# Optimization experiments

Measured on AMD Instinct MI355X. Metric: run time of the kernel, lower is better.

Reference implementation:

```python
import jax, jax.numpy as jnp
import numpy as np

B, N, D = 4, 4096, 1024
STD = 1.0 / D

def setup_inputs() -> dict:
    key = jax.random.key(0)
    ks = jax.random.split(key, 6)
    return {
        "x_real": jax.random.normal(ks[0], (B, N, D), dtype=jnp.float32),
        "x_imag": jax.random.normal(ks[1], (B, N, D), dtype=jnp.float32),
        "w_query_real": jax.random.normal(ks[2], (D, D), dtype=jnp.float32) * STD,
        "w_query_imag": jax.random.normal(ks[3], (D, D), dtype=jnp.float32) * STD,
        "w_key": jax.random.normal(ks[4], (D, D), dtype=jnp.float32) * STD,
        "w_value": jax.random.normal(ks[5], (D, D), dtype=jnp.float32) * STD,
    }

def reference(x_real, x_imag, w_query_real, w_query_imag, w_key, w_value):
    # query gate: (x.real @ Wqr) * (x.imag @ Wqi)  -> [b, n, e]
    query = jnp.einsum('bnd,de->bne', x_real, w_query_real) * \
            jnp.einsum('bnd,de->bne', x_imag, w_query_imag)
    key = jnp.einsum('bnd,de->bne', x_real, w_key)      # [b, n, d]
    value = jnp.einsum('bnd,de->bne', x_imag, w_value)  # [b, n, e]
    # linear-attention style reduction over sequence dim n
    kv_attn = jnp.einsum('bnd,bne->bde', key, value)    # [b, d, e]
    # dropout with p=0.0 (eval / identity)
    bffn = jnp.einsum('bnd,bde->bne', query, kv_attn)   # [b, n, e]
    return bffn
```

## Files before the change

### kernel.cpp

```cpp
#include <hip/hip_runtime.h>
#include <stdint.h>

typedef unsigned short ushort_t;
typedef __attribute__((ext_vector_type(8))) short bf16x8;
typedef __attribute__((ext_vector_type(4))) float f32x4;

__device__ __forceinline__ ushort_t f2bf(float f) {
  union { float f; uint32_t u; } v; v.f = f;
  uint32_t u = v.u;
  u += 0x7FFFu + ((u >> 16) & 1u);
  return (ushort_t)(u >> 16);
}
__device__ __forceinline__ float bf2f(ushort_t h) {
  union { uint32_t u; float f; } v; v.u = ((uint32_t)h) << 16;
  return v.f;
}
__device__ __forceinline__ void gl2lds16(const void* g, void* l) {
  __builtin_amdgcn_global_load_lds(
      (__attribute__((address_space(1))) void*)(uintptr_t)g,
      (__attribute__((address_space(3))) void*)(uint32_t)(uintptr_t)l,
      16, 0, 0);
}

__device__ __forceinline__ void gemm256x128(
    const ushort_t* __restrict__ A, int lda,
    const ushort_t* __restrict__ Bt, int ldb,
    int m0, int n0, int K, char* __restrict__ smem,
    f32x4 (&acc)[4][4]) {
  const int t = threadIdx.x;
  const int lane = t & 63, wid = t >> 6;
  const int wm = wid >> 1, wn = wid & 1;
  const int lr = lane & 15, lq = lane >> 4;
  const int nt = K >> 5;

  const int rowS = t >> 2;
  const int kgS = (t & 3) ^ ((t >> 3) & 3);
  const ushort_t* a0 = A + (size_t)(m0 + rowS) * lda + kgS * 8;
  const ushort_t* a1 = a0 + (size_t)128 * lda;
  const ushort_t* b0 = Bt + (size_t)(n0 + rowS) * ldb + kgS * 8;
  const int d0 = t * 16;

  const int o = lr * 64 + ((lq ^ ((lr >> 1) & 3)) << 4);
  const int aW = wm * 4096;
  const int bW = 16384 + wn * 4096;

#define STAGE(tt, buf) do { \
    char* s = smem + (buf); \
    gl2lds16(a0 + (tt) * 32, s + d0); \
    gl2lds16(a1 + (tt) * 32, s + 8192 + d0); \
    gl2lds16(b0 + (tt) * 32, s + 16384 + d0); \
  } while (0)

  bf16x8 aF[4], bF[4];

  STAGE(0, 0);
  for (int tt = 0; tt < nt; ++tt) {
    asm volatile("s_waitcnt vmcnt(0) lgkmcnt(0)\n\ts_barrier" ::: "memory");
    const int cb = (tt & 1) ? 24576 : 0;
    if (tt + 1 < nt) STAGE(tt + 1, (tt & 1) ? 0 : 24576);
    const char* base = smem + cb;
    #pragma unroll
    for (int mi = 0; mi < 4; ++mi)
      aF[mi] = *(const bf16x8*)(base + aW + mi * 1024 + o);
    #pragma unroll
    for (int ni = 0; ni < 4; ++ni)
      bF[ni] = *(const bf16x8*)(base + bW + ni * 1024 + o);
    __builtin_amdgcn_s_setprio(1);
    #pragma unroll
    for (int mi = 0; mi < 4; ++mi)
      #pragma unroll
      for (int ni = 0; ni < 4; ++ni)
        acc[mi][ni] = __builtin_amdgcn_mfma_f32_16x16x32_bf16(aF[mi], bF[ni], acc[mi][ni], 0, 0, 0);
    __builtin_amdgcn_s_setprio(0);
  }
#undef STAGE
}

template <bool GATE>
__global__ __launch_bounds__(512, 4) void proj8(
    const ushort_t* __restrict__ X, const ushort_t* __restrict__ Wt,
    ushort_t* __restrict__ Cq, ushort_t* __restrict__ Ct,
    const ushort_t* __restrict__ gate) {
  extern __shared__ char smem[];
  const int bid = blockIdx.x;
  const int xcd = bid & 7, i = bid >> 3;
  const int m0 = (xcd * 8 + (i >> 4)) * 256;
  const int n0 = (i & 15) * 128;
  f32x4 acc[4][4] = {};
  gemm256x128(X, 1024, Wt, 1024, m0, n0, 1024, smem, acc);

  const int t = threadIdx.x, lane = t & 63, wid = t >> 6;
  const int wm = wid >> 1, wn = wid & 1;
  const int lr = lane & 15, lq = lane >> 4;

  if (n0 < 1024) {
    #pragma unroll
    for (int mi = 0; mi < 4; ++mi) {
      int rbase = m0 + wm * 64 + mi * 16 + lq * 4;
      #pragma unroll
      for (int ni = 0; ni < 4; ++ni) {
        int c = n0 + wn * 64 + ni * 16 + lr;
        #pragma unroll
        for (int r = 0; r < 4; ++r) {
          float v = acc[mi][ni][r];
          if constexpr (GATE) v *= bf2f(gate[(size_t)(rbase + r) * 1024 + c]);
          Cq[(size_t)(rbase + r) * 1024 + c] = f2bf(v);
        }
      }
    }
  } else {
    const int b = m0 >> 12, nseq0 = m0 & 4095;
    #pragma unroll
    for (int p = 0; p < 2; ++p) {
      __syncthreads();
      #pragma unroll
      for (int mi = 0; mi < 4; ++mi) {
        int ns0 = wm * 64 + mi * 16 + lq * 4;
        int nc = ns0 >> 3, half8 = (ns0 >> 2) & 1;
        #pragma unroll
        for (int nib = 0; nib < 2; ++nib) {
          int ni = p * 2 + nib;
          int row = wn * 32 + nib * 16 + lr;
          ushort4 u = make_ushort4(f2bf(acc[mi][ni][0]), f2bf(acc[mi][ni][1]),
                                   f2bf(acc[mi][ni][2]), f2bf(acc[mi][ni][3]));
          *(ushort4*)(smem + row * 512 + ((nc ^ (row & 31)) * 16) + half8 * 8) = u;
        }
      }
      __syncthreads();
      #pragma unroll
      for (int j = 0; j < 4; ++j) {
        int g = j * 512 + t;
        int r = g >> 5, nc2 = g & 31;
        bf16x8 v = *(const bf16x8*)(smem + r * 512 + ((nc2 ^ (r & 31)) * 16));
        int d = n0 - 1024 + (r >> 5) * 64 + p * 32 + ((r >> 4) & 1) * 16 + (r & 15);
        *(bf16x8*)&Ct[(((size_t)(b * 1024 + d)) << 12) + nseq0 + nc2 * 8] = v;
      }
    }
  }
}

__global__ __launch_bounds__(512, 4) void kv8(
    const ushort_t* __restrict__ VT, const ushort_t* __restrict__ KT,
    ushort_t* __restrict__ P) {
  extern __shared__ char smem[];
  const int bid = blockIdx.x;
  const int xcd = bid & 7, i = bid >> 3;
  const int z = xcd * 2 + (i >> 5);
  const int mn = i & 31;
  const int m0 = (mn >> 3) * 256, n0 = (mn & 7) * 128;
  const int b = z & 3, s = z >> 2;
  const ushort_t* A = VT + ((size_t)b << 22) + s * 1024;
  const ushort_t* Bt = KT + ((size_t)b << 22) + s * 1024;
  f32x4 acc[4][4] = {};
  gemm256x128(A, 4096, Bt, 4096, m0, n0, 1024, smem, acc);

  const int t = threadIdx.x, lane = t & 63, wid = t >> 6;
  const int wm = wid >> 1, wn = wid & 1;
  const int lr = lane & 15, lq = lane >> 4;
  ushort_t* C = P + ((size_t)z << 20);
  #pragma unroll
  for (int mi = 0; mi < 4; ++mi) {
    int rbase = m0 + wm * 64 + mi * 16 + lq * 4;
    #pragma unroll
    for (int ni = 0; ni < 4; ++ni) {
      int c = n0 + wn * 64 + ni * 16 + lr;
      #pragma unroll
      for (int r = 0; r < 4; ++r)
        C[(size_t)(rbase + r) * 1024 + c] = f2bf(acc[mi][ni][r]);
    }
  }
}

__global__ __launch_bounds__(256) void kv_reduce(const ushort_t* __restrict__ P,
                                                 ushort_t* __restrict__ KVT) {
  size_t e4 = ((size_t)blockIdx.x * 256 + threadIdx.x) * 4;
  int b = (int)(e4 >> 20);
  size_t j = e4 & ((1u << 20) - 1);
  float s0 = 0.f, s1 = 0.f, s2 = 0.f, s3 = 0.f;
  #pragma unroll
  for (int sp = 0; sp < 4; ++sp) {
    ushort4 v = *(const ushort4*)(P + ((size_t)(sp * 4 + b) << 20) + j);
    s0 += bf2f(v.x); s1 += bf2f(v.y); s2 += bf2f(v.z); s3 += bf2f(v.w);
  }
  *(ushort4*)&KVT[e4] = make_ushort4(f2bf(s0), f2bf(s1), f2bf(s2), f2bf(s3));
}

__global__ __launch_bounds__(512, 4) void fin8(
    const ushort_t* __restrict__ Q, const ushort_t* __restrict__ KVT,
    float* __restrict__ Out) {
  extern __shared__ char smem[];
  const int bid = blockIdx.x;
  const int xcd = bid & 7, i = bid >> 3;
  const int m0 = (xcd * 8 + (i >> 3)) * 256;
  const int n0 = (i & 7) * 128;
  const int b = m0 >> 12;
  f32x4 acc[4][4] = {};
  gemm256x128(Q, 1024, KVT + ((size_t)b << 20), 1024, m0, n0, 1024, smem, acc);

  const int t = threadIdx.x, lane = t & 63, wid = t >> 6;
  const int wm = wid >> 1, wn = wid & 1;
  const int lr = lane & 15, lq = lane >> 4;
  #pragma unroll
  for (int mi = 0; mi < 4; ++mi) {
    int rbase = m0 + wm * 64 + mi * 16 + lq * 4;
    #pragma unroll
    for (int ni = 0; ni < 4; ++ni) {
      int c = n0 + wn * 64 + ni * 16 + lr;
      #pragma unroll
      for (int r = 0; r < 4; ++r)
        Out[(size_t)(rbase + r) * 1024 + c] = acc[mi][ni][r];
    }
  }
}

__global__ __launch_bounds__(256) void prep(
    const float* __restrict__ xr, const float* __restrict__ xi,
    const float* w0, const float* w1, const float* w2, const float* w3,
    ushort_t* __restrict__ xrb, ushort_t* __restrict__ xib,
    ushort_t* o0, ushort_t* o1, ushort_t* o2, ushort_t* o3) {
  const int bid = blockIdx.x;
  const int t = threadIdx.x;
  if (bid < 4096) {
    __shared__ float tile[32][33];
    const float* W; ushort_t* O;
    switch (bid >> 10) {
      case 0: W = w0; O = o0; break;
      case 1: W = w1; O = o1; break;
      case 2: W = w2; O = o2; break;
      default: W = w3; O = o3; break;
    }
    const int within = bid & 1023;
    const int bx = (within & 31) * 32, by = (within >> 5) * 32;
    const int tx = t & 31, ty = t >> 5;
    #pragma unroll
    for (int k = 0; k < 32; k += 8)
      tile[ty + k][tx] = W[(size_t)(by + ty + k) * 1024 + bx + tx];
    __syncthreads();
    #pragma unroll
    for (int k = 0; k < 32; k += 8)
      O[(size_t)(bx + ty + k) * 1024 + by + tx] = f2bf(tile[tx][ty + k]);
  } else {
    const size_t T = 16u * 1024u * 1024u;
    size_t e = ((size_t)(bid - 4096) * 256 + t) * 8;
    const float* src; ushort_t* dst;
    if (e < T) { src = xr + e; dst = xrb + e; }
    else       { src = xi + (e - T); dst = xib + (e - T); }
    float4 f0 = *(const float4*)src;
    float4 f1 = *(const float4*)(src + 4);
    ushort4 u0 = make_ushort4(f2bf(f0.x), f2bf(f0.y), f2bf(f0.z), f2bf(f0.w));
    ushort4 u1 = make_ushort4(f2bf(f1.x), f2bf(f1.y), f2bf(f1.z), f2bf(f1.w));
    *(ushort4*)dst = u0;
    *(ushort4*)(dst + 4) = u1;
  }
}

extern "C" void kernel_launch(void* const* d_in, const int* in_sizes, int n_in,
                              void* d_out, int out_size, void* d_ws, size_t ws_size,
                              hipStream_t stream) {
  const float* xr  = (const float*)d_in[0];
  const float* xi  = (const float*)d_in[1];
  const float* wqr = (const float*)d_in[2];
  const float* wqi = (const float*)d_in[3];
  const float* wk  = (const float*)d_in[4];
  const float* wv  = (const float*)d_in[5];

  char* ws = (char*)d_ws;
  const size_t MB = 1024ull * 1024ull;
  ushort_t* WtQR = (ushort_t*)(ws + 0 * MB);
  ushort_t* WtK  = (ushort_t*)(ws + 2 * MB);
  ushort_t* WtQI = (ushort_t*)(ws + 4 * MB);
  ushort_t* WtV  = (ushort_t*)(ws + 6 * MB);
  ushort_t* Xrb  = (ushort_t*)(ws + 8 * MB);
  ushort_t* Xib  = (ushort_t*)(ws + 40 * MB);
  ushort_t* KT   = (ushort_t*)(ws + 72 * MB);
  ushort_t* Q    = (ushort_t*)(ws + 104 * MB);
  ushort_t* VT   = (ushort_t*)(ws + 8 * MB);
  ushort_t* KVT  = (ushort_t*)(ws + 40 * MB);
  ushort_t* QR   = (ushort_t*)d_out;
  ushort_t* KVP  = (ushort_t*)d_out;

  static bool inited = false;
  if (!inited) {
    inited = true;
    hipFuncSetAttribute((const void*)&proj8<false>, hipFuncAttributeMaxDynamicSharedMemorySize, 49152);
    hipFuncSetAttribute((const void*)&proj8<true>,  hipFuncAttributeMaxDynamicSharedMemorySize, 49152);
    hipFuncSetAttribute((const void*)&kv8,          hipFuncAttributeMaxDynamicSharedMemorySize, 49152);
    hipFuncSetAttribute((const void*)&fin8,         hipFuncAttributeMaxDynamicSharedMemorySize, 49152);
  }

  prep<<<20480, 256, 0, stream>>>(xr, xi, wqr, wqi, wk, wv,
                                  Xrb, Xib, WtQR, WtQI, WtK, WtV);
  proj8<false><<<1024, 512, 49152, stream>>>(Xrb, WtQR, QR, KT, nullptr);
  proj8<true><<<1024, 512, 49152, stream>>>(Xib, WtQI, Q, VT, QR);
  kv8<<<512, 512, 49152, stream>>>(VT, KT, KVP);
  kv_reduce<<<4096, 256, 0, stream>>>(KVP, KVT);
  fin8<<<512, 512, 49152, stream>>>(Q, KVT, (float*)d_out);
}
```

Before: 420.4 us.

## Reassociate key-value product via Gram matrix of inputs and fuse query projections

Result: slower. 438.9 us (+4.4%).

```diff
diff --git a/kernel.cpp b/kernel.cpp
--- a/kernel.cpp
+++ b/kernel.cpp
@@ -22,24 +22,24 @@
       16, 0, 0);
 }
 
+
+template <bool F32OUT>
 __device__ __forceinline__ void gemm256x128(
     const ushort_t* __restrict__ A, int lda,
     const ushort_t* __restrict__ Bt, int ldb,
     int m0, int n0, int K, char* __restrict__ smem,
     f32x4 (&acc)[4][4]) {
   const int t = threadIdx.x;
-  const int lane = t & 63, wid = t >> 6;
-  const int wm = wid >> 1, wn = wid & 1;
-  const int lr = lane & 15, lq = lane >> 4;
   const int nt = K >> 5;
-
   const int rowS = t >> 2;
   const int kgS = (t & 3) ^ ((t >> 3) & 3);
   const ushort_t* a0 = A + (size_t)(m0 + rowS) * lda + kgS * 8;
   const ushort_t* a1 = a0 + (size_t)128 * lda;
   const ushort_t* b0 = Bt + (size_t)(n0 + rowS) * ldb + kgS * 8;
   const int d0 = t * 16;
-
+  const int lane = t & 63, wid = t >> 6;
+  const int wm = wid >> 1, wn = wid & 1;
+  const int lr = lane & 15, lq = lane >> 4;
   const int o = lr * 64 + ((lq ^ ((lr >> 1) & 3)) << 4);
   const int aW = wm * 4096;
   const int bW = 16384 + wn * 4096;
@@ -52,7 +52,6 @@
   } while (0)
 
   bf16x8 aF[4], bF[4];
-
   STAGE(0, 0);
   for (int tt = 0; tt < nt; ++tt) {
     asm volatile("s_waitcnt vmcnt(0) lgkmcnt(0)\n\ts_barrier" ::: "memory");
@@ -76,72 +75,90 @@
 #undef STAGE
 }
 
-template <bool GATE>
-__global__ __launch_bounds__(512, 4) void proj8(
-    const ushort_t* __restrict__ X, const ushort_t* __restrict__ Wt,
-    ushort_t* __restrict__ Cq, ushort_t* __restrict__ Ct,
-    const ushort_t* __restrict__ gate) {
+__global__ __launch_bounds__(512, 2) void gq(
+    const ushort_t* __restrict__ Xr, const ushort_t* __restrict__ Xi,
+    const ushort_t* __restrict__ Wr, const ushort_t* __restrict__ Wi,
+    ushort_t* __restrict__ Q) {
   extern __shared__ char smem[];
   const int bid = blockIdx.x;
   const int xcd = bid & 7, i = bid >> 3;
-  const int m0 = (xcd * 8 + (i >> 4)) * 256;
-  const int n0 = (i & 15) * 128;
-  f32x4 acc[4][4] = {};
-  gemm256x128(X, 1024, Wt, 1024, m0, n0, 1024, smem, acc);
-
-  const int t = threadIdx.x, lane = t & 63, wid = t >> 6;
+  const int m0 = (xcd * 8 + (i >> 3)) * 256;
+  const int n0 = (i & 7) * 128;
+  const int t = threadIdx.x;
+  const int lane = t & 63, wid = t >> 6;
   const int wm = wid >> 1, wn = wid & 1;
   const int lr = lane & 15, lq = lane >> 4;
 
-  if (n0 < 1024) {
+  const int rowS = t >> 2;
+  const int kgS = (t & 3) ^ ((t >> 3) & 3);
+  const ushort_t* ar0 = Xr + (size_t)(m0 + rowS) * 1024 + kgS * 8;
+  const ushort_t* ar1 = ar0 + (size_t)128 * 1024;
+  const ushort_t* ai0 = Xi + (size_t)(m0 + rowS) * 1024 + kgS * 8;
+  const ushort_t* ai1 = ai0 + (size_t)128 * 1024;
+  const ushort_t* br0 = Wr + (size_t)(n0 + rowS) * 1024 + kgS * 8;
+  const ushort_t* bi0 = Wi + (size_t)(n0 + rowS) * 1024 + kgS * 8;
+  const int d0 = t * 16;
+  const int o = lr * 64 + ((lq ^ ((lr >> 1) & 3)) << 4);
+  const int aW = wm * 4096;
+  const int bW = wn * 4096;
+
+#define STAGEQ(tt, buf) do { \
+    char* s = smem + (buf); \
+    gl2lds16(ar0 + (tt) * 32, s + d0); \
+    gl2lds16(ar1 + (tt) * 32, s + 8192 + d0); \
+    gl2lds16(ai0 + (tt) * 32, s + 16384 + d0); \
+    gl2lds16(ai1 + (tt) * 32, s + 24576 + d0); \
+    gl2lds16(br0 + (tt) * 32, s + 32768 + d0); \
+    gl2lds16(bi0 + (tt) * 32, s + 40960 + d0); \
+  } while (0)
+
+  f32x4 accR[4][4] = {}, accI[4][4] = {};
+  bf16x8 aR[4], aI[4], bR[4], bI[4];
+
+  STAGEQ(0, 0);
+  for (int tt = 0; tt < 32; ++tt) {
+    asm volatile("s_waitcnt vmcnt(0) lgkmcnt(0)\n\ts_barrier" ::: "memory");
+    const int cb = (tt & 1) ? 49152 : 0;
+    if (tt + 1 < 32) STAGEQ(tt + 1, (tt & 1) ? 0 : 49152);
+    const char* base = smem + cb;
     #pragma unroll
     for (int mi = 0; mi < 4; ++mi) {
-      int rbase = m0 + wm * 64 + mi * 16 + lq * 4;
+      aR[mi] = *(const bf16x8*)(base + aW + mi * 1024 + o);
+      aI[mi] = *(const bf16x8*)(base + 16384 + aW + mi * 1024 + o);
+    }
+    #pragma unroll
+    for (int ni = 0; ni < 4; ++ni) {
+      bR[ni] = *(const bf16x8*)(base + 32768 + bW + ni * 1024 + o);
+      bI[ni] = *(const bf16x8*)(base + 40960 + bW + ni * 1024 + o);
+    }
+    __builtin_amdgcn_s_setprio(1);
+    #pragma unroll
+    for (int mi = 0; mi < 4; ++mi)
       #pragma unroll
       for (int ni = 0; ni < 4; ++ni) {
-        int c = n0 + wn * 64 + ni * 16 + lr;
-        #pragma unroll
-        for (int r = 0; r < 4; ++r) {
-          float v = acc[mi][ni][r];
-          if constexpr (GATE) v *= bf2f(gate[(size_t)(rbase + r) * 1024 + c]);
-          Cq[(size_t)(rbase + r) * 1024 + c] = f2bf(v);
-        }
+        accR[mi][ni] = __builtin_amdgcn_mfma_f32_16x16x32_bf16(aR[mi], bR[ni], accR[mi][ni], 0, 0, 0);
+        accI[mi][ni] = __builtin_amdgcn_mfma_f32_16x16x32_bf16(aI[mi], bI[ni], accI[mi][ni], 0, 0, 0);
       }
-    }
-  } else {
-    const int b = m0 >> 12, nseq0 = m0 & 4095;
-    #pragma unroll
-    for (int p = 0; p < 2; ++p) {
-      __syncthreads();
-      #pragma unroll
-      for (int mi = 0; mi < 4; ++mi) {
-        int ns0 = wm * 64 + mi * 16 + lq * 4;
-        int nc = ns0 >> 3, half8 = (ns0 >> 2) & 1;
-        #pragma unroll
-        for (int nib = 0; nib < 2; ++nib) {
-          int ni = p * 2 + nib;
-          int row = wn * 32 + nib * 16 + lr;
-          ushort4 u = make_ushort4(f2bf(acc[mi][ni][0]), f2bf(acc[mi][ni][1]),
-                                   f2bf(acc[mi][ni][2]), f2bf(acc[mi][ni][3]));
-          *(ushort4*)(smem + row * 512 + ((nc ^ (row & 31)) * 16) + half8 * 8) = u;
-        }
-      }
-      __syncthreads();
-      #pragma unroll
-      for (int j = 0; j < 4; ++j) {
-        int g = j * 512 + t;
-        int r = g >> 5, nc2 = g & 31;
-        bf16x8 v = *(const bf16x8*)(smem + r * 512 + ((nc2 ^ (r & 31)) * 16));
-        int d = n0 - 1024 + (r >> 5) * 64 + p * 32 + ((r >> 4) & 1) * 16 + (r & 15);
-        *(bf16x8*)&Ct[(((size_t)(b * 1024 + d)) << 12) + nseq0 + nc2 * 8] = v;
-      }
-    }
-  }
-}
-
-__global__ __launch_bounds__(512, 4) void kv8(
-    const ushort_t* __restrict__ VT, const ushort_t* __restrict__ KT,
-    ushort_t* __restrict__ P) {
+    __builtin_amdgcn_s_setprio(0);
+  }
+#undef STAGEQ
+
+  #pragma unroll
+  for (int mi = 0; mi < 4; ++mi) {
+    int rbase = m0 + wm * 64 + mi * 16 + lq * 4;
+    #pragma unroll
+    for (int ni = 0; ni < 4; ++ni) {
+      int c = n0 + wn * 64 + ni * 16 + lr;
+      #pragma unroll
+      for (int r = 0; r < 4; ++r)
+        Q[(size_t)(rbase + r) * 1024 + c] = f2bf(accR[mi][ni][r] * accI[mi][ni][r]);
+    }
+  }
+}
+
+__global__ __launch_bounds__(512, 4) void gpart(
+    const ushort_t* __restrict__ XrT, const ushort_t* __restrict__ XiT,
+    float* __restrict__ P) {
   extern __shared__ char smem[];
   const int bid = blockIdx.x;
   const int xcd = bid & 7, i = bid >> 3;
@@ -149,15 +166,15 @@
   const int mn = i & 31;
   const int m0 = (mn >> 3) * 256, n0 = (mn & 7) * 128;
   const int b = z & 3, s = z >> 2;
-  const ushort_t* A = VT + ((size_t)b << 22) + s * 1024;
-  const ushort_t* Bt = KT + ((size_t)b << 22) + s * 1024;
+  const ushort_t* A = XrT + ((size_t)b << 22) + s * 1024;
+  const ushort_t* Bt = XiT + ((size_t)b << 22) + s * 1024;
   f32x4 acc[4][4] = {};
-  gemm256x128(A, 4096, Bt, 4096, m0, n0, 1024, smem, acc);
+  gemm256x128<true>(A, 4096, Bt, 4096, m0, n0, 1024, smem, acc);
 
   const int t = threadIdx.x, lane = t & 63, wid = t >> 6;
   const int wm = wid >> 1, wn = wid & 1;
   const int lr = lane & 15, lq = lane >> 4;
-  ushort_t* C = P + ((size_t)z << 20);
+  float* C = P + ((size_t)z << 20);
   #pragma unroll
   for (int mi = 0; mi < 4; ++mi) {
     int rbase = m0 + wm * 64 + mi * 16 + lq * 4;
@@ -166,23 +183,95 @@
       int c = n0 + wn * 64 + ni * 16 + lr;
       #pragma unroll
       for (int r = 0; r < 4; ++r)
-        C[(size_t)(rbase + r) * 1024 + c] = f2bf(acc[mi][ni][r]);
-    }
-  }
-}
-
-__global__ __launch_bounds__(256) void kv_reduce(const ushort_t* __restrict__ P,
-                                                 ushort_t* __restrict__ KVT) {
+        C[(size_t)(rbase + r) * 1024 + c] = acc[mi][ni][r];
+    }
+  }
+}
+
+__global__ __launch_bounds__(256) void g_reduce(const float* __restrict__ P,
+                                                ushort_t* __restrict__ G) {
   size_t e4 = ((size_t)blockIdx.x * 256 + threadIdx.x) * 4;
   int b = (int)(e4 >> 20);
   size_t j = e4 & ((1u << 20) - 1);
   float s0 = 0.f, s1 = 0.f, s2 = 0.f, s3 = 0.f;
   #pragma unroll
   for (int sp = 0; sp < 4; ++sp) {
-    ushort4 v = *(const ushort4*)(P + ((size_t)(sp * 4 + b) << 20) + j);
-    s0 += bf2f(v.x); s1 += bf2f(v.y); s2 += bf2f(v.z); s3 += bf2f(v.w);
-  }
-  *(ushort4*)&KVT[e4] = make_ushort4(f2bf(s0), f2bf(s1), f2bf(s2), f2bf(s3));
+    float4 v = *(const float4*)(P + ((size_t)(sp * 4 + b) << 20) + j);
+    s0 += v.x; s1 += v.y; s2 += v.z; s3 += v.w;
+  }
+  *(ushort4*)&G[e4] = make_ushort4(f2bf(s0), f2bf(s1), f2bf(s2), f2bf(s3));
+}
+
+__global__ __launch_bounds__(256, 4) void gemm1k(
+    const ushort_t* __restrict__ Abase, int aStride,
+    const ushort_t* __restrict__ Btbase, int btStride,
+    ushort_t* __restrict__ Cbase) {
+  extern __shared__ char smem[];
+  const int bid = blockIdx.x;
+  const int b = bid >> 6, mn = bid & 63;
+  const int m0 = (mn >> 3) * 128, n0 = (mn & 7) * 128;
+  const ushort_t* A = Abase + (size_t)b * (size_t)aStride;
+  const ushort_t* Bt = Btbase + (size_t)b * (size_t)btStride;
+
+  const int t = threadIdx.x;
+  const int lane = t & 63, wid = t >> 6;
+  const int wm = wid >> 1, wn = wid & 1;
+  const int lr = lane & 15, lq = lane >> 4;
+  const int rowS = t >> 2;
+  const int kgS = (t & 3) ^ ((t >> 3) & 3);
+  const ushort_t* a0 = A + (size_t)(m0 + rowS) * 1024 + kgS * 8;
+  const ushort_t* a1 = a0 + (size_t)64 * 1024;
+  const ushort_t* b0 = Bt + (size_t)(n0 + rowS) * 1024 + kgS * 8;
+  const ushort_t* b1 = b0 + (size_t)64 * 1024;
+  const int d0 = t * 16, d1 = 4096 + t * 16;
+  const int o = lr * 64 + ((lq ^ ((lr >> 1) & 3)) << 4);
+  const int aW = wm * 4096;
+  const int bW = 8192 + wn * 4096;
+
+#define STG1(tt, buf) do { \
+    char* s = smem + (buf); \
+    gl2lds16(a0 + (tt) * 32, s + d0); \
+    gl2lds16(a1 + (tt) * 32, s + d1); \
+    gl2lds16(b0 + (tt) * 32, s + 8192 + d0); \
+    gl2lds16(b1 + (tt) * 32, s + 8192 + d1); \
+  } while (0)
+
+  f32x4 acc[4][4] = {};
+  bf16x8 aF[4], bF[4];
+  STG1(0, 0);
+  for (int tt = 0; tt < 32; ++tt) {
+    asm volatile("s_waitcnt vmcnt(0) lgkmcnt(0)\n\ts_barrier" ::: "memory");
+    const int cb = (tt & 1) ? 16384 : 0;
+    if (tt + 1 < 32) STG1(tt + 1, (tt & 1) ? 0 : 16384);
+    const char* base = smem + cb;
+    #pragma unroll
+    for (int mi = 0; mi < 4; ++mi)
+      aF[mi] = *(const bf16x8*)(base + aW + mi * 1024 + o);
+    #pragma unroll
+    for (int ni = 0; ni < 4; ++ni)
+      bF[ni] = *(const bf16x8*)(base + bW + ni * 1024 + o);
+    __builtin_amdgcn_s_setprio(1);
+    #pragma unroll
+    for (int mi = 0; mi < 4; ++mi)
+      #pragma unroll
+      for (int ni = 0; ni < 4; ++ni)
+        acc[mi][ni] = __builtin_amdgcn_mfma_f32_16x16x32_bf16(aF[mi], bF[ni], acc[mi][ni], 0, 0, 0);
+    __builtin_amdgcn_s_setprio(0);
+  }
+#undef STG1
+
+  ushort_t* C = Cbase + ((size_t)b << 20);
+  #pragma unroll
+  for (int mi = 0; mi < 4; ++mi) {
+    int rbase = m0 + wm * 64 + mi * 16 + lq * 4;
+    #pragma unroll
+    for (int ni = 0; ni < 4; ++ni) {
+      int c = n0 + wn * 64 + ni * 16 + lr;
+      #pragma unroll
+      for (int r = 0; r < 4; ++r)
+        C[(size_t)(rbase + r) * 1024 + c] = f2bf(acc[mi][ni][r]);
+    }
+  }
 }
 
 __global__ __launch_bounds__(512, 4) void fin8(
@@ -195,7 +284,7 @@
   const int n0 = (i & 7) * 128;
   const int b = m0 >> 12;
   f32x4 acc[4][4] = {};
-  gemm256x128(Q, 1024, KVT + ((size_t)b << 20), 1024, m0, n0, 1024, smem, acc);
+  gemm256x128<true>(Q, 1024, KVT + ((size_t)b << 20), 1024, m0, n0, 1024, smem, acc);
 
   const int t = threadIdx.x, lane = t & 63, wid = t >> 6;
   const int wm = wid >> 1, wn = wid & 1;
@@ -213,15 +302,17 @@
   }
 }
 
-__global__ __launch_bounds__(256) void prep(
+__global__ __launch_bounds__(256) void prep2(
     const float* __restrict__ xr, const float* __restrict__ xi,
     const float* w0, const float* w1, const float* w2, const float* w3,
     ushort_t* __restrict__ xrb, ushort_t* __restrict__ xib,
+    ushort_t* __restrict__ xrT, ushort_t* __restrict__ xiT,
     ushort_t* o0, ushort_t* o1, ushort_t* o2, ushort_t* o3) {
   const int bid = blockIdx.x;
   const int t = threadIdx.x;
+  __shared__ float tile[32][33];
+  const int tx = t & 31, ty = t >> 5;
   if (bid < 4096) {
-    __shared__ float tile[32][33];
     const float* W; ushort_t* O;
     switch (bid >> 10) {
       case 0: W = w0; O = o0; break;
@@ -231,7 +322,6 @@
     }
     const int within = bid & 1023;
     const int bx = (within & 31) * 32, by = (within >> 5) * 32;
-    const int tx = t & 31, ty = t >> 5;
     #pragma unroll
     for (int k = 0; k < 32; k += 8)
       tile[ty + k][tx] = W[(size_t)(by + ty + k) * 1024 + bx + tx];
@@ -240,17 +330,27 @@
     for (int k = 0; k < 32; k += 8)
       O[(size_t)(bx + ty + k) * 1024 + by + tx] = f2bf(tile[tx][ty + k]);
   } else {
-    const size_t T = 16u * 1024u * 1024u;
-    size_t e = ((size_t)(bid - 4096) * 256 + t) * 8;
-    const float* src; ushort_t* dst;
-    if (e < T) { src = xr + e; dst = xrb + e; }
-    else       { src = xi + (e - T); dst = xib + (e - T); }
-    float4 f0 = *(const float4*)src;
-    float4 f1 = *(const float4*)(src + 4);
-    ushort4 u0 = make_ushort4(f2bf(f0.x), f2bf(f0.y), f2bf(f0.z), f2bf(f0.w));
-    ushort4 u1 = make_ushort4(f2bf(f1.x), f2bf(f1.y), f2bf(f1.z), f2bf(f1.w));
-    *(ushort4*)dst = u0;
-    *(ushort4*)(dst + 4) = u1;
+    const int xb = bid - 4096;
+    const int tensor = xb >> 14;
+    const int within = xb & 16383;
+    const int by = (within >> 5) * 32;
+    const int bx = (within & 31) * 32;
+    const float* src = tensor ? xi : xr;
+    ushort_t* dstS = tensor ? xib : xrb;
+    ushort_t* dstT = tensor ? xiT : xrT;
+    #pragma unroll
+    for (int k = 0; k < 32; k += 8) {
+      float v = src[(size_t)(by + ty + k) * 1024 + bx + tx];
+      tile[ty + k][tx] = v;
+      dstS[(size_t)(by + ty + k) * 1024 + bx + tx] = f2bf(v);
+    }
+    __syncthreads();
+    const int b = by >> 12;
+    const int nn = by & 4095;
+    #pragma unroll
+    for (int k = 0; k < 32; k += 8)
+      dstT[((size_t)b << 22) + (size_t)(bx + ty + k) * 4096 + nn + tx] =
+          f2bf(tile[tx][ty + k]);
   }
 }
 
@@ -267,32 +367,34 @@
   char* ws = (char*)d_ws;
   const size_t MB = 1024ull * 1024ull;
   ushort_t* WtQR = (ushort_t*)(ws + 0 * MB);
-  ushort_t* WtK  = (ushort_t*)(ws + 2 * MB);
-  ushort_t* WtQI = (ushort_t*)(ws + 4 * MB);
+  ushort_t* WtQI = (ushort_t*)(ws + 2 * MB);
+  ushort_t* WtK  = (ushort_t*)(ws + 4 * MB);
   ushort_t* WtV  = (ushort_t*)(ws + 6 * MB);
-  ushort_t* Xrb  = (ushort_t*)(ws + 8 * MB);
-  ushort_t* Xib  = (ushort_t*)(ws + 40 * MB);
-  ushort_t* KT   = (ushort_t*)(ws + 72 * MB);
-  ushort_t* Q    = (ushort_t*)(ws + 104 * MB);
-  ushort_t* VT   = (ushort_t*)(ws + 8 * MB);
-  ushort_t* KVT  = (ushort_t*)(ws + 40 * MB);
-  ushort_t* QR   = (ushort_t*)d_out;
-  ushort_t* KVP  = (ushort_t*)d_out;
+  ushort_t* XrT  = (ushort_t*)(ws + 8 * MB);
+  ushort_t* XiT  = (ushort_t*)(ws + 40 * MB);
+  ushort_t* Q    = (ushort_t*)(ws + 72 * MB);
+  ushort_t* G    = (ushort_t*)(ws + 104 * MB);
+  ushort_t* H    = (ushort_t*)(ws + 8 * MB);
+  ushort_t* KVT  = (ushort_t*)(ws + 16 * MB);
+  ushort_t* Xrb  = (ushort_t*)d_out;
+  ushort_t* Xib  = (ushort_t*)((char*)d_out + 32 * MB);
+  float*    Pf   = (float*)d_out;
 
   static bool inited = false;
   if (!inited) {
     inited = true;
-    hipFuncSetAttribute((const void*)&proj8<false>, hipFuncAttributeMaxDynamicSharedMemorySize, 49152);
-    hipFuncSetAttribute((const void*)&proj8<true>,  hipFuncAttributeMaxDynamicSharedMemorySize, 49152);
-    hipFuncSetAttribute((const void*)&kv8,          hipFuncAttributeMaxDynamicSharedMemorySize, 49152);
-    hipFuncSetAttribute((const void*)&fin8,         hipFuncAttributeMaxDynamicSharedMemorySize, 49152);
-  }
-
-  prep<<<20480, 256, 0, stream>>>(xr, xi, wqr, wqi, wk, wv,
-                                  Xrb, Xib, WtQR, WtQI, WtK, WtV);
-  proj8<false><<<1024, 512, 49152, stream>>>(Xrb, WtQR, QR, KT, nullptr);
-  proj8<true><<<1024, 512, 49152, stream>>>(Xib, WtQI, Q, VT, QR);
-  kv8<<<512, 512, 49152, stream>>>(VT, KT, KVP);
-  kv_reduce<<<4096, 256, 0, stream>>>(KVP, KVT);
+    hipFuncSetAttribute((const void*)&gq,     hipFuncAttributeMaxDynamicSharedMemorySize, 98304);
+    hipFuncSetAttribute((const void*)&gpart,  hipFuncAttributeMaxDynamicSharedMemorySize, 49152);
+    hipFuncSetAttribute((const void*)&gemm1k, hipFuncAttributeMaxDynamicSharedMemorySize, 32768);
+    hipFuncSetAttribute((const void*)&fin8,   hipFuncAttributeMaxDynamicSharedMemorySize, 49152);
+  }
+
+  prep2<<<36864, 256, 0, stream>>>(xr, xi, wqr, wqi, wk, wv,
+                                   Xrb, Xib, XrT, XiT, WtQR, WtQI, WtK, WtV);
+  gq<<<512, 512, 98304, stream>>>(Xrb, Xib, WtQR, WtQI, Q);
+  gpart<<<512, 512, 49152, stream>>>(XrT, XiT, Pf);
+  g_reduce<<<4096, 256, 0, stream>>>(Pf, G);
+  gemm1k<<<256, 256, 32768, stream>>>(WtV, 0, G, 1 << 20, H);
+  gemm1k<<<256, 256, 32768, stream>>>(H, 1 << 20, WtK, 0, KVT);
   fin8<<<512, 512, 49152, stream>>>(Q, KVT, (float*)d_out);
 }
```
